# Kernel tuning notes

Hardware: AMD Instinct MI355X
Metric: run time of the kernel (lower is better)

Reference implementation:

```python
import jax, jax.numpy as jnp
from jax import lax
import numpy as np

W = 64  # window_size

def setup_inputs() -> dict:
    key = jax.random.key(0)
    x = jax.random.normal(key, (262144, 32), dtype=jnp.float32)
    return {"x": x}

def _roll(x, init, op):
    # sliding window of size W along axis 0, stride 1, VALID -> (T-W+1, F)
    return lax.reduce_window(x, init, op, window_dimensions=(W, 1),
                             window_strides=(1, 1), padding="VALID")

def reference(x):
    # drop_na=True, stride=1, keep_original=False,
    # statistics = [mean, std, min, max, sum] concatenated on last axis.
    s = _roll(x, jnp.float32(0), lax.add)          # rolling sum
    s2 = _roll(x * x, jnp.float32(0), lax.add)     # rolling sum of squares
    mean = s / W
    # tf.math.reduce_std is population std: sqrt(E[x^2] - E[x]^2)
    std = jnp.sqrt(jnp.maximum(s2 / W - mean * mean, 0.0))
    mn = _roll(x, jnp.float32(jnp.inf), lax.min)
    mx = _roll(x, jnp.float32(-jnp.inf), lax.max)
    return jnp.concatenate([mean, std, mn, mx, s], axis=-1)
```

## Files before the change

kernel.cpp:

```cpp
#include <hip/hip_runtime.h>
#include <math.h>


#define WINW 64
#define RCH 16
#define NF 32
#define CHUNKS_PER_BLK 8
#define ROWS_PER_BLK (CHUNKS_PER_BLK * RCH)
#define STAGE_ROWS (ROWS_PER_BLK + WINW)

__global__ __launch_bounds__(256, 4) void rolling_stats_kernel(
    const float* __restrict__ x, float* __restrict__ out, int N, int T_out) {
  __shared__ float tile[STAGE_ROWS * NF];

  int t0_blk = blockIdx.x * ROWS_PER_BLK;

  const float4* xv = (const float4*)x;
  float4* tv = (float4*)tile;
#pragma unroll
  for (int it = 0; it < (STAGE_ROWS * NF / 4) / 256; ++it) {
    int f = it * 256 + (int)threadIdx.x;
    int r = f >> 3;
    int gr = t0_blk + r;
    gr = gr < N ? gr : N - 1;
    tv[f] = xv[(size_t)gr * (NF / 4) + (f & 7)];
  }
  __syncthreads();

  int c = (int)threadIdx.x & (NF - 1);
  int lr0 = ((int)threadIdx.x >> 5) * RCH;
  int t0 = t0_blk + lr0;
  const float* tc = tile + c;

  float smin[RCH], smax[RCH];
  float ssum = 0.f, ssq = 0.f;
  float rmin = INFINITY, rmax = -INFINITY;

#pragma unroll
  for (int j = WINW - 1; j >= RCH; --j) {
    float a = tc[(lr0 + j) * NF];
    rmin = fminf(rmin, a);
    rmax = fmaxf(rmax, a);
    ssum += a;
    ssq = fmaf(a, a, ssq);
  }
#pragma unroll
  for (int j = RCH - 1; j >= 0; --j) {
    float a = tc[(lr0 + j) * NF];
    rmin = fminf(rmin, a);
    rmax = fmaxf(rmax, a);
    ssum += a;
    ssq = fmaf(a, a, ssq);
    smin[j] = rmin;
    smax[j] = rmax;
  }

  float pmin = INFINITY, pmax = -INFINITY;
  float wsum = ssum, wsq = ssq;
  float* o = out + (size_t)t0 * (5 * NF) + c;
#pragma unroll
  for (int j = 0; j < RCH; ++j) {
    if (j > 0) {
      float bnew = tc[(lr0 + WINW - 1 + j) * NF];
      float aold = tc[(lr0 + j - 1) * NF];
      pmin = fminf(pmin, bnew);
      pmax = fmaxf(pmax, bnew);
      wsum += bnew - aold;
      wsq = fmaf(bnew, bnew, wsq);
      wsq = fmaf(-aold, aold, wsq);
    }
    if (t0 + j < T_out) {
      float wmin = fminf(smin[j], pmin);
      float wmax = fmaxf(smax[j], pmax);
      float mean = wsum * 0.015625f;
      float var = fmaf(-mean, mean, wsq * 0.015625f);
      var = fmaxf(var, 0.f);
      float sd = sqrtf(var);
      float* orow = o + (size_t)j * (5 * NF);
      orow[0 * NF] = mean;
      orow[1 * NF] = sd;
      orow[2 * NF] = wmin;
      orow[3 * NF] = wmax;
      orow[4 * NF] = wsum;
    }
  }
}

extern "C" void kernel_launch(void* const* d_in, const int* in_sizes, int n_in,
                              void* d_out, int out_size, void* d_ws,
                              size_t ws_size, hipStream_t stream) {
  const float* x = (const float*)d_in[0];
  float* out = (float*)d_out;
  int N = in_sizes[0] / NF;
  int T_out = N - (WINW - 1);
  int nblocks = (T_out + ROWS_PER_BLK - 1) / ROWS_PER_BLK;
  rolling_stats_kernel<<<nblocks, 256, 0, stream>>>(x, out, N, T_out);
}
```

Measured before the change: 185.1 us.

## Process two tiles per block with register-prefetched next tile loads

Each block now handles two consecutive 128-row tiles. While computing the current tile from shared memory, it holds the next tile's global loads in registers (float4 g[6]) so the fetch overlaps with compute. Launch bounds drop from 4 to 3 blocks per SM to make room for the extra registers. This halves the block count and may reduce occupancy. Halo rows are still reloaded per tile.

Result: slower. 197.8 us (+6.8%).

```diff
diff --git a/kernel.cpp b/kernel.cpp
--- a/kernel.cpp
+++ b/kernel.cpp
@@ -5,83 +5,110 @@
 #define WINW 64
 #define RCH 16
 #define NF 32
-#define CHUNKS_PER_BLK 8
-#define ROWS_PER_BLK (CHUNKS_PER_BLK * RCH)
-#define STAGE_ROWS (ROWS_PER_BLK + WINW)
+#define CHUNKS 8
+#define TROWS (CHUNKS * RCH)
+#define SROWS (TROWS + WINW)
+#define FVT (SROWS * NF / 4 / 256)
+#define TILES_PER_BLK 2
 
-__global__ __launch_bounds__(256, 4) void rolling_stats_kernel(
-    const float* __restrict__ x, float* __restrict__ out, int N, int T_out) {
-  __shared__ float tile[STAGE_ROWS * NF];
+__global__ __launch_bounds__(256, 3) void rolling_stats_kernel(
+    const float* __restrict__ x, float* __restrict__ out, int N, int T_out,
+    int ntiles) {
+  __shared__ float tile[SROWS * NF];
+  float4* tv = (float4*)tile;
+  const float4* xv = (const float4*)x;
 
-  int t0_blk = blockIdx.x * ROWS_PER_BLK;
+  int tid = (int)threadIdx.x;
+  int c = tid & (NF - 1);
+  int lr0 = (tid >> 5) * RCH;
 
-  const float4* xv = (const float4*)x;
-  float4* tv = (float4*)tile;
+  float4 g[FVT];
+  int t = blockIdx.x * TILES_PER_BLK;
+
+  {
+    int base = t * TROWS;
 #pragma unroll
-  for (int it = 0; it < (STAGE_ROWS * NF / 4) / 256; ++it) {
-    int f = it * 256 + (int)threadIdx.x;
-    int r = f >> 3;
-    int gr = t0_blk + r;
-    gr = gr < N ? gr : N - 1;
-    tv[f] = xv[(size_t)gr * (NF / 4) + (f & 7)];
+    for (int i = 0; i < FVT; ++i) {
+      int f = i * 256 + tid;
+      int gr = base + (f >> 3);
+      gr = gr < N ? gr : N - 1;
+      g[i] = xv[(size_t)gr * (NF / 4) + (f & 7)];
+    }
   }
-  __syncthreads();
-
-  int c = (int)threadIdx.x & (NF - 1);
-  int lr0 = ((int)threadIdx.x >> 5) * RCH;
-  int t0 = t0_blk + lr0;
-  const float* tc = tile + c;
-
-  float smin[RCH], smax[RCH];
-  float ssum = 0.f, ssq = 0.f;
-  float rmin = INFINITY, rmax = -INFINITY;
 
 #pragma unroll
-  for (int j = WINW - 1; j >= RCH; --j) {
-    float a = tc[(lr0 + j) * NF];
-    rmin = fminf(rmin, a);
-    rmax = fmaxf(rmax, a);
-    ssum += a;
-    ssq = fmaf(a, a, ssq);
-  }
+  for (int it = 0; it < TILES_PER_BLK; ++it, ++t) {
+    if (t >= ntiles) break;
+    __syncthreads();
 #pragma unroll
-  for (int j = RCH - 1; j >= 0; --j) {
-    float a = tc[(lr0 + j) * NF];
-    rmin = fminf(rmin, a);
-    rmax = fmaxf(rmax, a);
-    ssum += a;
-    ssq = fmaf(a, a, ssq);
-    smin[j] = rmin;
-    smax[j] = rmax;
-  }
+    for (int i = 0; i < FVT; ++i) tv[i * 256 + tid] = g[i];
 
-  float pmin = INFINITY, pmax = -INFINITY;
-  float wsum = ssum, wsq = ssq;
-  float* o = out + (size_t)t0 * (5 * NF) + c;
+    if (it + 1 < TILES_PER_BLK && t + 1 < ntiles) {
+      int base = (t + 1) * TROWS;
 #pragma unroll
-  for (int j = 0; j < RCH; ++j) {
-    if (j > 0) {
-      float bnew = tc[(lr0 + WINW - 1 + j) * NF];
-      float aold = tc[(lr0 + j - 1) * NF];
-      pmin = fminf(pmin, bnew);
-      pmax = fmaxf(pmax, bnew);
-      wsum += bnew - aold;
-      wsq = fmaf(bnew, bnew, wsq);
-      wsq = fmaf(-aold, aold, wsq);
+      for (int i = 0; i < FVT; ++i) {
+        int f = i * 256 + tid;
+        int gr = base + (f >> 3);
+        gr = gr < N ? gr : N - 1;
+        g[i] = xv[(size_t)gr * (NF / 4) + (f & 7)];
+      }
     }
-    if (t0 + j < T_out) {
-      float wmin = fminf(smin[j], pmin);
-      float wmax = fmaxf(smax[j], pmax);
-      float mean = wsum * 0.015625f;
-      float var = fmaf(-mean, mean, wsq * 0.015625f);
-      var = fmaxf(var, 0.f);
-      float sd = sqrtf(var);
-      float* orow = o + (size_t)j * (5 * NF);
-      orow[0 * NF] = mean;
-      orow[1 * NF] = sd;
-      orow[2 * NF] = wmin;
-      orow[3 * NF] = wmax;
-      orow[4 * NF] = wsum;
+    __syncthreads();
+
+    const float* tc = tile + c;
+    int t0 = t * TROWS + lr0;
+
+    float smin[RCH], smax[RCH];
+    float ssum = 0.f, ssq = 0.f;
+    float rmin = INFINITY, rmax = -INFINITY;
+
+#pragma unroll
+    for (int j = WINW - 1; j >= RCH; --j) {
+      float a = tc[(lr0 + j) * NF];
+      rmin = fminf(rmin, a);
+      rmax = fmaxf(rmax, a);
+      ssum += a;
+      ssq = fmaf(a, a, ssq);
+    }
+#pragma unroll
+    for (int j = RCH - 1; j >= 0; --j) {
+      float a = tc[(lr0 + j) * NF];
+      rmin = fminf(rmin, a);
+      rmax = fmaxf(rmax, a);
+      ssum += a;
+      ssq = fmaf(a, a, ssq);
+      smin[j] = rmin;
+      smax[j] = rmax;
+    }
+
+    float pmin = INFINITY, pmax = -INFINITY;
+    float wsum = ssum, wsq = ssq;
+    float* o = out + (size_t)t0 * (5 * NF) + c;
+#pragma unroll
+    for (int j = 0; j < RCH; ++j) {
+      if (j > 0) {
+        float bnew = tc[(lr0 + WINW - 1 + j) * NF];
+        float aold = tc[(lr0 + j - 1) * NF];
+        pmin = fminf(pmin, bnew);
+        pmax = fmaxf(pmax, bnew);
+        wsum += bnew - aold;
+        wsq = fmaf(bnew, bnew, wsq);
+        wsq = fmaf(-aold, aold, wsq);
+      }
+      if (t0 + j < T_out) {
+        float wmin = fminf(smin[j], pmin);
+        float wmax = fmaxf(smax[j], pmax);
+        float mean = wsum * 0.015625f;
+        float var = fmaf(-mean, mean, wsq * 0.015625f);
+        var = fmaxf(var, 0.f);
+        float sd = sqrtf(var);
+        float* orow = o + (size_t)j * (5 * NF);
+        orow[0 * NF] = mean;
+        orow[1 * NF] = sd;
+        orow[2 * NF] = wmin;
+        orow[3 * NF] = wmax;
+        orow[4 * NF] = wsum;
+      }
     }
   }
 }
@@ -93,6 +120,7 @@
   float* out = (float*)d_out;
   int N = in_sizes[0] / NF;
   int T_out = N - (WINW - 1);
-  int nblocks = (T_out + ROWS_PER_BLK - 1) / ROWS_PER_BLK;
-  rolling_stats_kernel<<<nblocks, 256, 0, stream>>>(x, out, N, T_out);
+  int ntiles = (T_out + TROWS - 1) / TROWS;
+  int nblocks = (ntiles + TILES_PER_BLK - 1) / TILES_PER_BLK;
+  rolling_stats_kernel<<<nblocks, 256, 0, stream>>>(x, out, N, T_out, ntiles);
 }
```
